# Optimization experiments

Measured on AMD Instinct MI355X. Metric: run time of the kernel, lower is better.

The kernel has to match this reference:

```python
import jax, jax.numpy as jnp
import numpy as np

B, C, L = 64, 128, 1024
SCALES = [8, 4, 2, 1]
EPS_BN = 1e-5


def _ema_vec(x_ds, alpha):
    # x_ds: [B, C, Ls]; alpha: [1, C, 1] in (0,1)
    Ls = x_ds.shape[-1]
    powers = jnp.arange(Ls - 1, -1, -1, dtype=x_ds.dtype)
    base = jnp.power(1.0 - alpha, powers)                                 # [1, C, Ls]
    w_num = jnp.concatenate([base[..., :1], base[..., 1:] * alpha], axis=-1)
    num = jnp.cumsum(x_ds * w_num, axis=-1)
    den = jnp.maximum(jnp.cumsum(base, axis=-1), 1e-12)
    return num / den


def _dwconv(x, w, s):
    # depthwise Conv1d: kernel 2s, stride s, pad s//2, groups=C, no bias
    return jax.lax.conv_general_dilated(
        x, w, window_strides=(s,), padding=[(s // 2, s // 2)],
        dimension_numbers=("NCH", "OIH", "NCH"), feature_group_count=C)


def _proj(v, w1, b1, w2, b2):
    # v: [B, C, Ls] -> Linear(Ls->L), exact GELU, Linear(L->L); torch Linear y = x @ W.T + b
    h = jax.nn.gelu(jnp.einsum("bcs,ls->bcl", v, w1) + b1, approximate=False)
    return jnp.einsum("bcl,ml->bcm", h, w2) + b2


def _hasd(x, bn_g, bn_b, branch, gate):
    Bn = x.shape[0]
    # BatchNorm1d over flattened (C*L) features, training-mode batch stats (biased var)
    v = x.reshape(Bn, C * L)
    mu = v.mean(axis=0)
    var = jnp.mean((v - mu) ** 2, axis=0)
    xn = (((v - mu) / jnp.sqrt(var + EPS_BN)) * bn_g + bn_b).reshape(Bn, C, L)
    trends, seasons, gates = [], [], []
    for s in SCALES:
        if s > 1:
            cw, w1, b1, w2, b2 = branch[s]
            down = _dwconv(xn, cw, s)                                     # [B, C, L//s]
            up = _proj(down, w1, b1, w2, b2)                              # [B, C, L]
        else:
            down = xn
            up = xn
        gw, gb, al = gate[s]
        alpha = jax.nn.sigmoid(al)
        trend_ds = _ema_vec(down, alpha)
        trend_up = _proj(trend_ds, w1, b1, w2, b2) if s > 1 else trend_ds
        season = up - trend_up
        trends.append(trend_up)
        seasons.append(season)
        gates.append(jax.nn.sigmoid(season.mean(axis=-1) @ gw.T + gb))    # [B, 1]
    g = jnp.concatenate(gates, axis=1)                                    # [B, n_scales]
    g = g / (g.sum(axis=1, keepdims=True) + 1e-6)
    g = g[:, :, None, None]
    trend_out = (jnp.stack(trends, axis=1) * g).sum(axis=1)
    season_out = (jnp.stack(seasons, axis=1) * g).sum(axis=1)
    return season_out, trend_out


def setup_inputs() -> dict:
    key = jax.random.key(0)
    ks = iter(jax.random.split(key, 64))
    d = {"x": jax.random.normal(next(ks), (B, C, L), jnp.float32)}
    d["bn_g"] = 1.0 + 0.1 * jax.random.normal(next(ks), (C * L,), jnp.float32)
    d["bn_b"] = 0.1 * jax.random.normal(next(ks), (C * L,), jnp.float32)
    for s in (8, 4, 2):
        Ls = L // s
        d[f"cw{s}"] = jax.random.normal(next(ks), (C, 1, 2 * s), jnp.float32) / np.sqrt(2 * s)
        d[f"w1_{s}"] = jax.random.normal(next(ks), (L, Ls), jnp.float32) / np.sqrt(Ls)
        d[f"b1_{s}"] = jnp.zeros((L,), jnp.float32)
        d[f"w2_{s}"] = jax.random.normal(next(ks), (L, L), jnp.float32) / np.sqrt(L)
        d[f"b2_{s}"] = jnp.zeros((L,), jnp.float32)
    for s in SCALES:
        d[f"gw{s}"] = jax.random.normal(next(ks), (1, C), jnp.float32) / np.sqrt(C)
        d[f"gb{s}"] = jnp.zeros((1,), jnp.float32)
        d[f"al{s}"] = jnp.full((1, C, 1), 0.3, jnp.float32)
    return d


def reference(x, bn_g, bn_b,
              cw8, w1_8, b1_8, w2_8, b2_8,
              cw4, w1_4, b1_4, w2_4, b2_4,
              cw2, w1_2, b1_2, w2_2, b2_2,
              gw8, gb8, al8, gw4, gb4, al4, gw2, gb2, al2, gw1, gb1, al1):
    branch = {8: (cw8, w1_8, b1_8, w2_8, b2_8),
              4: (cw4, w1_4, b1_4, w2_4, b2_4),
              2: (cw2, w1_2, b1_2, w2_2, b2_2)}
    gate = {8: (gw8, gb8, al8), 4: (gw4, gb4, al4),
            2: (gw2, gb2, al2), 1: (gw1, gb1, al1)}
    return _hasd(x, bn_g, bn_b, branch, gate)
```

## Files before the change

kernel.cpp:

```cpp
#include <hip/hip_runtime.h>
#include <hip/hip_bf16.h>
#include <math.h>

#define Bdim 64
#define Cdim 128
#define Ldim 1024
#define BC   (Bdim * Cdim)
#define CLn  (Cdim * Ldim)
#define TOT  (Bdim * CLn)

typedef unsigned short ushort_t;
typedef short s16x8 __attribute__((ext_vector_type(8)));
typedef float f32x4 __attribute__((ext_vector_type(4)));

__device__ __forceinline__ float bf2f(ushort_t u) {
    return __uint_as_float(((unsigned)u) << 16);
}
__device__ __forceinline__ ushort_t f2bf(float f) {
    __hip_bfloat16 h = __float2bfloat16(f);
    return *(ushort_t*)&h;
}
__device__ __forceinline__ void async16(const ushort_t* g, ushort_t* l) {
    __builtin_amdgcn_global_load_lds(
        (const __attribute__((address_space(1))) unsigned int*)g,
        (__attribute__((address_space(3))) unsigned int*)l, 16, 0, 0);
}
__device__ __forceinline__ float fast_gelu(float z) {
    float z2 = z * z;
    float inner = fmaf(0.044715f * z2, z, z);
    float e = __expf(-1.5957691216057308f * inner);
    return z * __builtin_amdgcn_rcpf(1.f + e);
}

__global__ __launch_bounds__(256) void bn_stats_kernel(
    const float* __restrict__ x, const float* __restrict__ bn_g,
    const float* __restrict__ bn_b, float* __restrict__ scale,
    float* __restrict__ shift)
{
    int f = blockIdx.x * 256 + threadIdx.x;
    float sum = 0.f, sumsq = 0.f;
    for (int b = 0; b < Bdim; ++b) {
        float v = x[(size_t)b * CLn + f];
        sum += v; sumsq += v * v;
    }
    float mu  = sum * (1.f / Bdim);
    float var = fmaxf(sumsq * (1.f / Bdim) - mu * mu, 0.f);
    float sc  = bn_g[f] / sqrtf(var + 1e-5f);
    scale[f] = sc;
    shift[f] = bn_b[f] - mu * sc;
}

__global__ __launch_bounds__(256) void convert_weights_kernel(
    const float* __restrict__ w1_8, const float* __restrict__ w1_4,
    const float* __restrict__ w1_2, const float* __restrict__ w2_8,
    const float* __restrict__ w2_4, const float* __restrict__ w2_2,
    ushort_t* __restrict__ dst)
{
    int idx = blockIdx.x * 256 + threadIdx.x;
    const float* src; int off;
    if      (idx < 131072)  { src = w1_8; off = 0; }
    else if (idx < 393216)  { src = w1_4; off = 131072; }
    else if (idx < 917504)  { src = w1_2; off = 393216; }
    else if (idx < 1966080) { src = w2_8; off = 917504; }
    else if (idx < 3014656) { src = w2_4; off = 1966080; }
    else                    { src = w2_2; off = 3014656; }
    dst[idx] = f2bf(src[idx - off]);
}

__global__ __launch_bounds__(256) void w2colsum_kernel(
    const float* __restrict__ w2_8, const float* __restrict__ w2_4,
    const float* __restrict__ w2_2, float* __restrict__ w2cs)
{
    const float* w = (blockIdx.y == 0) ? w2_8 : (blockIdx.y == 1) ? w2_4 : w2_2;
    int h  = blockIdx.x * 64 + (threadIdx.x & 63);
    int ls = threadIdx.x >> 6;
    float s = 0.f;
    for (int l = ls; l < 1024; l += 4) s += w[(size_t)l * 1024 + h];
    __shared__ float red[4][64];
    red[ls][threadIdx.x & 63] = s;
    __syncthreads();
    if (ls == 0)
        w2cs[blockIdx.y * 1024 + h] =
            red[0][threadIdx.x] + red[1][threadIdx.x] +
            red[2][threadIdx.x] + red[3][threadIdx.x];
}

__global__ __launch_bounds__(256) void ema_coef_kernel(
    const float* __restrict__ al1, const float* __restrict__ al2,
    const float* __restrict__ al4, const float* __restrict__ al8,
    float* __restrict__ coef, float* __restrict__ am)
{
    int c   = blockIdx.x;
    int tid = threadIdx.x;
    const float* als[4] = {al1, al2, al4, al8};
    const int Lss[4]    = {1024, 512, 256, 128};
    const int offs[4]   = {0, 1024, 1536, 1792};
#pragma unroll
    for (int si = 0; si < 4; ++si) {
        double a  = 1.0 / (1.0 + exp(-(double)als[si][c]));
        double m  = 1.0 - a;
        double lm = log(m);
        int Ls = Lss[si];
        for (int t = tid; t < Ls; t += 256) {
            double dt  = (1.0 - exp((double)(t + 1) * lm)) / a;
            double den = exp((double)(Ls - 1 - t) * lm) * dt;
            double ramp = (den >= 1e-12) ? 1.0 : den * 1e12;
            coef[(size_t)c * 1920 + offs[si] + t] = (float)(ramp / dt);
        }
        if (tid == 0) {
            am[c * 8 + si * 2 + 0] = (float)a;
            am[c * 8 + si * 2 + 1] = (float)m;
        }
    }
}

template<int SEG>
__device__ __forceinline__ void ema_pass1(
    const float* __restrict__ src, float a, float m, bool lead,
    float* __restrict__ xs, float& Sp, float& Sm)
{
    int lane = threadIdx.x & 63;
    if constexpr (SEG >= 4) {
#pragma unroll
        for (int i = 0; i < SEG; i += 4) {
            f32x4 u = *(const f32x4*)&src[lane * SEG + i];
            xs[i + 0] = u.x; xs[i + 1] = u.y;
            xs[i + 2] = u.z; xs[i + 3] = u.w;
        }
    } else {
        float2 u = *(const float2*)&src[lane * 2];
        xs[0] = u.x; xs[1] = u.y;
    }
    float p = 0.f;
#pragma unroll
    for (int i = 0; i < SEG; ++i) {
        float bi = a * xs[i];
        if (lead && lane == 0 && i == 0) bi = xs[0];
        p = fmaf(m, p, bi);
    }
    float sm = m;
#pragma unroll
    for (int i = 1; i < SEG; ++i) sm *= m;
    Sp = p; Sm = sm;
#pragma unroll
    for (int d = 1; d < 64; d <<= 1) {
        float pm = __shfl_up(Sp, d);
        float mm = __shfl_up(Sm, d);
        if (lane >= d) { Sp = fmaf(Sm, pm, Sp); Sm *= mm; }
    }
}

template<int SEG, bool DIFF>
__device__ __forceinline__ float ema_pass2(
    const float* __restrict__ xs, float a, float m, bool lead, float carry,
    const float* __restrict__ cf, ushort_t* __restrict__ dst)
{
    int lane = threadIdx.x & 63;
    float y = carry, diff = 0.f;
    unsigned pk[(SEG + 1) / 2];
#pragma unroll
    for (int i = 0; i < SEG; ++i) {
        float bi = a * xs[i];
        if (lead && lane == 0 && i == 0) bi = xs[0];
        y = fmaf(m, y, bi);
        float tr = y * cf[lane * SEG + i];
        unsigned h = f2bf(tr);
        if ((i & 1) == 0) pk[i >> 1] = h;
        else              pk[i >> 1] |= h << 16;
        if (DIFF) diff += xs[i] - tr;
    }
    if constexpr (SEG == 8) {
        uint4 v; v.x = pk[0]; v.y = pk[1]; v.z = pk[2]; v.w = pk[3];
        *(uint4*)(dst + lane * 8) = v;
    } else if constexpr (SEG == 4) {
        uint2 v; v.x = pk[0]; v.y = pk[1];
        *(uint2*)(dst + lane * 4) = v;
    } else {
        *(unsigned*)(dst + lane * 2) = pk[0];
    }
    return diff;
}

__global__ __launch_bounds__(256) void pre_kernel(
    const float* __restrict__ x, const float* __restrict__ scale,
    const float* __restrict__ shift,
    const float* __restrict__ cw8, const float* __restrict__ cw4,
    const float* __restrict__ cw2,
    const float* __restrict__ coef, const float* __restrict__ amtab,
    ushort_t* __restrict__ xn_bf, ushort_t* __restrict__ t1_bf,
    ushort_t* __restrict__ A8, ushort_t* __restrict__ A4,
    ushort_t* __restrict__ A2, float* __restrict__ rs)
{
    __shared__ float sxn[1024];
    __shared__ float sxnp[1056];
    __shared__ float sconv[896];
    __shared__ float sP0;
    __shared__ float sdiff[2];
    int r   = blockIdx.x;
    int c   = r & (Cdim - 1);
    int tid = threadIdx.x;

    {
        const float* xr = x + (size_t)r * 1024;
        float4 xv = *(const float4*)(xr + tid * 4);
        float4 sc = *(const float4*)(scale + (size_t)c * 1024 + tid * 4);
        float4 sh = *(const float4*)(shift + (size_t)c * 1024 + tid * 4);
        float v0 = fmaf(xv.x, sc.x, sh.x);
        float v1 = fmaf(xv.y, sc.y, sh.y);
        float v2 = fmaf(xv.z, sc.z, sh.z);
        float v3 = fmaf(xv.w, sc.w, sh.w);
        int p = tid * 4;
        sxn[p + 0] = v0; sxn[p + 1] = v1; sxn[p + 2] = v2; sxn[p + 3] = v3;
        int pp = p + (p >> 5);
        sxnp[pp + 0] = v0; sxnp[pp + 1] = v1;
        sxnp[pp + 2] = v2; sxnp[pp + 3] = v3;
        uint2 pk;
        pk.x = (unsigned)f2bf(v0) | ((unsigned)f2bf(v1) << 16);
        pk.y = (unsigned)f2bf(v2) | ((unsigned)f2bf(v3) << 16);
        *(uint2*)(xn_bf + (size_t)r * 1024 + tid * 4) = pk;
    }
    __syncthreads();

    {
        const float* w2 = cw2 + c * 4;
        unsigned a2pk = 0;
#pragma unroll
        for (int j = 0; j < 2; ++j) {
            int o = tid * 2 + j;
            int start = o * 2 - 1;
            float acc = 0.f;
#pragma unroll
            for (int k = 0; k < 4; ++k) {
                int pos = start + k;
                float v = (pos >= 0 && pos < 1024) ? sxnp[pos + (pos >> 5)] : 0.f;
                acc = fmaf(v, w2[k], acc);
            }
            sconv[o] = acc;
            a2pk |= ((unsigned)f2bf(acc)) << (j * 16);
        }
        *(unsigned*)(A2 + (size_t)r * 512 + tid * 2) = a2pk;
        {
            const float* w4 = cw4 + c * 8;
            int o = tid;
            int start = o * 4 - 2;
            float acc = 0.f;
#pragma unroll
            for (int k = 0; k < 8; ++k) {
                int pos = start + k;
                float v = (pos >= 0 && pos < 1024) ? sxnp[pos + (pos >> 5)] : 0.f;
                acc = fmaf(v, w4[k], acc);
            }
            sconv[512 + o] = acc;
            A4[(size_t)r * 256 + o] = f2bf(acc);
        }
        if (tid < 128) {
            const float* w8 = cw8 + c * 16;
            int o = tid;
            int start = o * 8 - 4;
            float acc = 0.f;
#pragma unroll
            for (int k = 0; k < 16; ++k) {
                int pos = start + k;
                float v = (pos >= 0 && pos < 1024) ? sxnp[pos + (pos >> 5)] : 0.f;
                acc = fmaf(v, w8[k], acc);
            }
            sconv[768 + o] = acc;
            A8[(size_t)r * 128 + o] = f2bf(acc);
        }
    }
    __syncthreads();

    int wave = tid >> 6;
    int lane = tid & 63;
    const float* cf = coef + (size_t)c * 1920;
    const float* am = amtab + c * 8;
    float xs[8];
    float Sp = 0.f, Sm = 1.f, aE = 0.f, mE = 0.f;

    if (wave == 0) {
        aE = am[0]; mE = am[1];
        ema_pass1<8>(sxn, aE, mE, true, xs, Sp, Sm);
        if (lane == 63) sP0 = Sp;
    } else if (wave == 1) {
        aE = am[0]; mE = am[1];
        ema_pass1<8>(sxn + 512, aE, mE, false, xs, Sp, Sm);
    } else if (wave == 2) {
        aE = am[2]; mE = am[3];
        ema_pass1<8>(sconv, aE, mE, true, xs, Sp, Sm);
    } else {
        aE = am[4]; mE = am[5];
        ema_pass1<4>(sconv + 512, aE, mE, true, xs, Sp, Sm);
    }
    __syncthreads();

    float cs  = __shfl_up(Sp, 1);
    float msf = __shfl_up(Sm, 1);
    float carry = lane ? cs : 0.f;

    if (wave == 0) {
        float d = ema_pass2<8, true>(xs, aE, mE, true, carry,
                                     cf, t1_bf + (size_t)r * 1024);
#pragma unroll
        for (int dd = 32; dd; dd >>= 1) d += __shfl_down(d, dd);
        if (lane == 0) sdiff[0] = d;
    } else if (wave == 1) {
        carry += sP0 * (lane ? msf : 1.f);
        float d = ema_pass2<8, true>(xs, aE, mE, false, carry,
                                     cf + 512, t1_bf + (size_t)r * 1024 + 512);
#pragma unroll
        for (int dd = 32; dd; dd >>= 1) d += __shfl_down(d, dd);
        if (lane == 0) sdiff[1] = d;
    } else if (wave == 2) {
        ema_pass2<8, false>(xs, aE, mE, true, carry,
                            cf + 1024, A2 + ((size_t)BC + r) * 512);
    } else {
        ema_pass2<4, false>(xs, aE, mE, true, carry,
                            cf + 1536, A4 + ((size_t)BC + r) * 256);
        float xs2[2];
        aE = am[6]; mE = am[7];
        ema_pass1<2>(sconv + 768, aE, mE, true, xs2, Sp, Sm);
        float cs2 = __shfl_up(Sp, 1);
        float c2  = lane ? cs2 : 0.f;
        ema_pass2<2, false>(xs2, aE, mE, true, c2,
                            cf + 1792, A8 + ((size_t)BC + r) * 128);
    }
    __syncthreads();
    if (tid == 0) rs[3 * BC + r] = sdiff[0] + sdiff[1];
}

__global__ __launch_bounds__(256, 2) void gemm1_kernel(
    const ushort_t* __restrict__ Abase,
    const ushort_t* __restrict__ Wbase,
    const float* __restrict__ b1_8, const float* __restrict__ b1_4,
    const float* __restrict__ b1_2, const float* __restrict__ w2cs,
    ushort_t* __restrict__ Hbase, float* __restrict__ rs)
{
    __shared__ ushort_t smem[24576];
    int gx = blockIdx.x;
    int z  = 2 - (gx >> 6);
    int mi = gx & 63;
    int K  = 128 << z;
    int NT = K >> 5;
    const ushort_t* A  = Abase + (size_t)2 * BC * 128 * ((1 << z) - 1);
    const ushort_t* Bw = Wbase + (size_t)131072 * ((1 << z) - 1);
    const float* bias  = (z == 0) ? b1_8 : (z == 1) ? b1_4 : b1_2;
    ushort_t* Hout     = Hbase + (size_t)z * 2 * TOT;

    int tid  = threadIdx.x;
    int wave = tid >> 6;
    int lane = tid & 63;
    int m0 = mi * 128, n0 = blockIdx.y * 128;
    int wm = (wave & 1) * 64, wn = (wave >> 1) * 64;
    int rlow = lane >> 2;
    int s4   = lane & 3;
    int fr   = lane & 15;
    int quad = lane >> 4;

    f32x4 accu[4][4], acct[4][4];
#pragma unroll
    for (int i = 0; i < 4; ++i)
#pragma unroll
        for (int j = 0; j < 4; ++j) {
            accu[i][j] = (f32x4){0.f, 0.f, 0.f, 0.f};
            acct[i][j] = (f32x4){0.f, 0.f, 0.f, 0.f};
        }

    auto stage = [&](int t, int buf) {
        int k0 = t * 32;
        ushort_t* base = smem + buf * 12288;
#pragma unroll
        for (int i = 0; i < 2; ++i) {
            int rb  = wave * 32 + i * 16;
            int row = rb + rlow;
            int cg  = (s4 - (row >> 1)) & 3;
            async16(A  + (size_t)(m0 + row) * K + k0 + cg * 8,      base + rb * 32);
            async16(A  + (size_t)(BC + m0 + row) * K + k0 + cg * 8, base + 4096 + rb * 32);
            async16(Bw + (size_t)(n0 + row) * K + k0 + cg * 8,      base + 8192 + rb * 32);
        }
    };

    stage(0, 0);
    int cur = 0;
    for (int t = 0; t < NT; ++t) {
        if (t + 1 < NT) {
            stage(t + 1, cur ^ 1);
            asm volatile("s_waitcnt vmcnt(6)" ::: "memory");
        } else {
            asm volatile("s_waitcnt vmcnt(0)" ::: "memory");
        }
        __builtin_amdgcn_s_barrier();
        __builtin_amdgcn_sched_barrier(0);
        const ushort_t* Au_ = smem + cur * 12288;
        const ushort_t* At_ = Au_ + 4096;
        const ushort_t* Bs_ = Au_ + 8192;
        s16x8 afu[4], aft[4], bfr[4];
#pragma unroll
        for (int q = 0; q < 4; ++q) {
            int nr = wn + q * 16 + fr;
            bfr[q] = *(const s16x8*)&Bs_[nr * 32 + ((quad + (nr >> 1)) & 3) * 8];
            int mr = wm + q * 16 + fr;
            afu[q] = *(const s16x8*)&Au_[mr * 32 + ((quad + (mr >> 1)) & 3) * 8];
            aft[q] = *(const s16x8*)&At_[mr * 32 + ((quad + (mr >> 1)) & 3) * 8];
        }
        __builtin_amdgcn_s_setprio(1);
#pragma unroll
        for (int mt = 0; mt < 4; ++mt)
#pragma unroll
            for (int nt = 0; nt < 4; ++nt)
                accu[mt][nt] = __builtin_amdgcn_mfma_f32_16x16x32_bf16(
                    afu[mt], bfr[nt], accu[mt][nt], 0, 0, 0);
#pragma unroll
        for (int mt = 0; mt < 4; ++mt)
#pragma unroll
            for (int nt = 0; nt < 4; ++nt)
                acct[mt][nt] = __builtin_amdgcn_mfma_f32_16x16x32_bf16(
                    aft[mt], bfr[nt], acct[mt][nt], 0, 0, 0);
        __builtin_amdgcn_s_setprio(0);
        __builtin_amdgcn_sched_barrier(0);
        __builtin_amdgcn_s_barrier();
        cur ^= 1;
    }

    float racc[16];
#pragma unroll
    for (int e = 0; e < 16; ++e) racc[e] = 0.f;
#pragma unroll
    for (int mt = 0; mt < 4; ++mt)
#pragma unroll
        for (int nt = 0; nt < 4; ++nt) {
            int col = n0 + wn + nt * 16 + fr;
            float bcol = bias[col];
            float wcs = w2cs[z * 1024 + col];
#pragma unroll
            for (int rr = 0; rr < 4; ++rr) {
                size_t row = m0 + wm + mt * 16 + quad * 4 + rr;
                float gu = fast_gelu(accu[mt][nt][rr] + bcol);
                float gt = fast_gelu(acct[mt][nt][rr] + bcol);
                Hout[row * 1024 + col]        = f2bf(gu);
                Hout[(BC + row) * 1024 + col] = f2bf(gt);
                racc[mt * 4 + rr] = fmaf(gu - gt, wcs, racc[mt * 4 + rr]);
            }
        }
#pragma unroll
    for (int e = 0; e < 16; ++e) {
        float v = racc[e];
        v += __shfl_xor(v, 1); v += __shfl_xor(v, 2);
        v += __shfl_xor(v, 4); v += __shfl_xor(v, 8);
        if (fr == 0) {
            int mt = e >> 2, rr = e & 3;
            int row = m0 + wm + mt * 16 + quad * 4 + rr;
            atomicAdd(&rs[z * BC + row], v);
        }
    }
}

__global__ __launch_bounds__(256, 2) void gemm2_kernel(
    const ushort_t* __restrict__ Hbase,
    const ushort_t* __restrict__ W2base,
    const float* __restrict__ b2_8, const float* __restrict__ b2_4,
    const float* __restrict__ b2_2, const float* __restrict__ g,
    const ushort_t* __restrict__ t1_bf, const ushort_t* __restrict__ xn_bf,
    float* __restrict__ trend_out, float* __restrict__ season_out)
{
    __shared__ ushort_t smem[24576];
    int tid  = threadIdx.x;
    int wave = tid >> 6;
    int lane = tid & 63;
    int m0 = blockIdx.x * 128, n0 = blockIdx.y * 128;
    int wm = (wave & 1) * 64, wn = (wave >> 1) * 64;
    int rlow = lane >> 2;
    int s4   = lane & 3;
    int fr   = lane & 15;
    int quad = lane >> 4;
    int b = m0 >> 7;
    float gv0 = g[b * 4 + 0], gv1 = g[b * 4 + 1], gv2 = g[b * 4 + 2];
    float g1  = g[b * 4 + 3];
    float gsv[3] = {gv0, gv1, gv2};

    f32x4 accu[4][4], acct[4][4];
#pragma unroll
    for (int i = 0; i < 4; ++i)
#pragma unroll
        for (int j = 0; j < 4; ++j) {
            accu[i][j] = (f32x4){0.f, 0.f, 0.f, 0.f};
            acct[i][j] = (f32x4){0.f, 0.f, 0.f, 0.f};
        }

    auto stage = [&](int kt, int buf) {
        int s  = kt >> 5;
        int k0 = (kt & 31) * 32;
        const ushort_t* Au = Hbase + (size_t)s * 2 * TOT;
        const ushort_t* At = Au + TOT;
        const ushort_t* Bw = W2base + (size_t)s * 1048576;
        ushort_t* base = smem + buf * 12288;
#pragma unroll
        for (int i = 0; i < 2; ++i) {
            int rb  = wave * 32 + i * 16;
            int row = rb + rlow;
            int cg  = (s4 - (row >> 1)) & 3;
            size_t goff = (size_t)(m0 + row) * 1024 + k0 + cg * 8;
            async16(Au + goff, base + rb * 32);
            async16(At + goff, base + 4096 + rb * 32);
            async16(Bw + (size_t)(n0 + row) * 1024 + k0 + cg * 8,
                    base + 8192 + rb * 32);
        }
    };

    stage(0, 0);
    int cur = 0;
    for (int kt = 0; kt < 96; ++kt) {
        if (kt + 1 < 96) {
            stage(kt + 1, cur ^ 1);
            asm volatile("s_waitcnt vmcnt(6)" ::: "memory");
        } else {
            asm volatile("s_waitcnt vmcnt(0)" ::: "memory");
        }
        __builtin_amdgcn_s_barrier();
        __builtin_amdgcn_sched_barrier(0);
        if (kt > 0 && (kt & 31) == 0) {
            int s = kt >> 5;
            float rr_ = gsv[s - 1] / fmaxf(gsv[s], 1e-30f);
#pragma unroll
            for (int mt = 0; mt < 4; ++mt)
#pragma unroll
                for (int nt = 0; nt < 4; ++nt)
#pragma unroll
                    for (int rr = 0; rr < 4; ++rr) {
                        accu[mt][nt][rr] *= rr_;
                        acct[mt][nt][rr] *= rr_;
                    }
        }
        const ushort_t* Au_ = smem + cur * 12288;
        const ushort_t* At_ = Au_ + 4096;
        const ushort_t* Bs_ = Au_ + 8192;
        s16x8 afu[4], aft[4], bfr[4];
#pragma unroll
        for (int q = 0; q < 4; ++q) {
            int nr = wn + q * 16 + fr;
            bfr[q] = *(const s16x8*)&Bs_[nr * 32 + ((quad + (nr >> 1)) & 3) * 8];
            int mr = wm + q * 16 + fr;
            afu[q] = *(const s16x8*)&Au_[mr * 32 + ((quad + (mr >> 1)) & 3) * 8];
            aft[q] = *(const s16x8*)&At_[mr * 32 + ((quad + (mr >> 1)) & 3) * 8];
        }
        __builtin_amdgcn_s_setprio(1);
#pragma unroll
        for (int mt = 0; mt < 4; ++mt)
#pragma unroll
            for (int nt = 0; nt < 4; ++nt)
                accu[mt][nt] = __builtin_amdgcn_mfma_f32_16x16x32_bf16(
                    afu[mt], bfr[nt], accu[mt][nt], 0, 0, 0);
#pragma unroll
        for (int mt = 0; mt < 4; ++mt)
#pragma unroll
            for (int nt = 0; nt < 4; ++nt)
                acct[mt][nt] = __builtin_amdgcn_mfma_f32_16x16x32_bf16(
                    aft[mt], bfr[nt], acct[mt][nt], 0, 0, 0);
        __builtin_amdgcn_s_setprio(0);
        __builtin_amdgcn_sched_barrier(0);
        __builtin_amdgcn_s_barrier();
        cur ^= 1;
    }
#pragma unroll
    for (int mt = 0; mt < 4; ++mt)
#pragma unroll
        for (int nt = 0; nt < 4; ++nt)
#pragma unroll
            for (int rr = 0; rr < 4; ++rr) {
                accu[mt][nt][rr] *= gv2;
                acct[mt][nt][rr] *= gv2;
            }

#pragma unroll
    for (int mt = 0; mt < 4; ++mt)
#pragma unroll
        for (int nt = 0; nt < 4; ++nt) {
            int col = n0 + wn + nt * 16 + fr;
            float cb2 = gv0 * b2_8[col] + gv1 * b2_4[col] + gv2 * b2_2[col];
#pragma unroll
            for (int r = 0; r < 4; ++r) {
                size_t row = m0 + wm + mt * 16 + quad * 4 + r;
                size_t idx = row * 1024 + col;
                float tr = acct[mt][nt][r] + cb2 + g1 * bf2f(t1_bf[idx]);
                float se = accu[mt][nt][r] + cb2 + g1 * bf2f(xn_bf[idx]) - tr;
                trend_out[idx]  = tr;
                season_out[idx] = se;
            }
        }
}

__global__ __launch_bounds__(128) void gate_kernel(
    const float* __restrict__ rs,
    const float* __restrict__ gw8, const float* __restrict__ gb8,
    const float* __restrict__ gw4, const float* __restrict__ gb4,
    const float* __restrict__ gw2, const float* __restrict__ gb2,
    const float* __restrict__ gw1, const float* __restrict__ gb1,
    float* __restrict__ g)
{
    int b = blockIdx.x;
    int c = threadIdx.x;
    const float* gws[4] = {gw8, gw4, gw2, gw1};
    const float* gbs[4] = {gb8, gb4, gb2, gb1};
    __shared__ float buf[128];
    __shared__ float gates[4];
    for (int si = 0; si < 4; ++si) {
        buf[c] = rs[si * BC + b * Cdim + c] * (1.f / Ldim) * gws[si][c];
        __syncthreads();
        for (int off = 64; off >= 1; off >>= 1) {
            if (c < off) buf[c] += buf[c + off];
            __syncthreads();
        }
        if (c == 0) {
            float z = buf[0] + gbs[si][0];
            gates[si] = 1.f / (1.f + expf(-z));
        }
        __syncthreads();
    }
    if (c == 0) {
        float s = gates[0] + gates[1] + gates[2] + gates[3] + 1e-6f;
#pragma unroll
        for (int si = 0; si < 4; ++si) g[b * 4 + si] = gates[si] / s;
    }
}

extern "C" void kernel_launch(void* const* d_in, const int* in_sizes, int n_in,
                              void* d_out, int out_size, void* d_ws, size_t ws_size,
                              hipStream_t stream)
{
    const float* x    = (const float*)d_in[0];
    const float* bn_g = (const float*)d_in[1];
    const float* bn_b = (const float*)d_in[2];
    const float* cw8  = (const float*)d_in[3];
    const float* w1_8 = (const float*)d_in[4];
    const float* b1_8 = (const float*)d_in[5];
    const float* w2_8 = (const float*)d_in[6];
    const float* b2_8 = (const float*)d_in[7];
    const float* cw4  = (const float*)d_in[8];
    const float* w1_4 = (const float*)d_in[9];
    const float* b1_4 = (const float*)d_in[10];
    const float* w2_4 = (const float*)d_in[11];
    const float* b2_4 = (const float*)d_in[12];
    const float* cw2  = (const float*)d_in[13];
    const float* w1_2 = (const float*)d_in[14];
    const float* b1_2 = (const float*)d_in[15];
    const float* w2_2 = (const float*)d_in[16];
    const float* b2_2 = (const float*)d_in[17];
    const float* gw8  = (const float*)d_in[18];
    const float* gb8  = (const float*)d_in[19];
    const float* al8  = (const float*)d_in[20];
    const float* gw4  = (const float*)d_in[21];
    const float* gb4  = (const float*)d_in[22];
    const float* al4  = (const float*)d_in[23];
    const float* gw2  = (const float*)d_in[24];
    const float* gb2  = (const float*)d_in[25];
    const float* al2  = (const float*)d_in[26];
    const float* gw1  = (const float*)d_in[27];
    const float* gb1  = (const float*)d_in[28];
    const float* al1  = (const float*)d_in[29];

    ushort_t* p_xn  = (ushort_t*)d_ws;
    ushort_t* p_t1  = p_xn + TOT;
    ushort_t* p_H   = p_t1 + TOT;
    ushort_t* p_wb  = p_H + 6 * (size_t)TOT;
    ushort_t* p_w1b = p_wb;
    ushort_t* p_w2b = p_wb + 917504;
    float*    p_sc  = (float*)(p_wb + 4063232);
    float*    p_sh  = p_sc + CLn;
    float*    p_w2cs = p_sh + CLn;
    float*    p_rs  = p_w2cs + 3 * 1024;
    float*    p_g   = p_rs + 4 * BC;
    float*    p_coef = (float*)p_H;
    float*    p_am   = p_coef + 128 * 1920;
    ushort_t* p_A8 = (ushort_t*)d_out;
    ushort_t* p_A4 = p_A8 + 2 * (size_t)BC * 128;
    ushort_t* p_A2 = p_A4 + 2 * (size_t)BC * 256;
    float*    p_season = (float*)d_out;
    float*    p_trend  = (float*)d_out + TOT;

    hipMemsetAsync(p_rs, 0, 4 * BC * sizeof(float), stream);
    bn_stats_kernel<<<CLn / 256, 256, 0, stream>>>(x, bn_g, bn_b, p_sc, p_sh);
    ema_coef_kernel<<<128, 256, 0, stream>>>(al1, al2, al4, al8, p_coef, p_am);
    convert_weights_kernel<<<4063232 / 256, 256, 0, stream>>>(
        w1_8, w1_4, w1_2, w2_8, w2_4, w2_2, p_wb);
    w2colsum_kernel<<<dim3(16, 3), 256, 0, stream>>>(w2_8, w2_4, w2_2, p_w2cs);

    pre_kernel<<<BC, 256, 0, stream>>>(x, p_sc, p_sh, cw8, cw4, cw2,
                                       p_coef, p_am,
                                       p_xn, p_t1, p_A8, p_A4, p_A2, p_rs);

    gemm1_kernel<<<dim3(192, 8), 256, 0, stream>>>(
        p_A8, p_w1b, b1_8, b1_4, b1_2, p_w2cs, p_H, p_rs);

    gate_kernel<<<Bdim, 128, 0, stream>>>(p_rs, gw8, gb8, gw4, gb4,
                                          gw2, gb2, gw1, gb1, p_g);

    gemm2_kernel<<<dim3(64, 8), 256, 0, stream>>>(
        p_H, p_w2b, b2_8, b2_4, b2_2, p_g, p_t1, p_xn, p_trend, p_season);
}
```

Before: 434.5 us.

## Load GEMM A-operand fragments straight from global into registers, stage only B in LDS

Both GEMM kernels stop staging the A operands (u and t activations) through LDS. Each wave now loads its MFMA fragments directly from global memory into registers, two steps ahead, and only the shared weight tile B goes through async LDS copies. LDS use drops from 48KB to 16KB per block and the A-tile LDS reads are removed. In exchange, A reads hit global memory without reuse across waves (the two N-waves load the same rows), the kernel holds more registers for double-buffered fragments, and the vmcnt wait logic becomes more fragile.

```diff
diff --git a/kernel.cpp b/kernel.cpp
--- a/kernel.cpp
+++ b/kernel.cpp
@@ -328,6 +328,41 @@
     if (tid == 0) rs[3 * BC + r] = sdiff[0] + sdiff[1];
 }
 
+#define MFMA_STEP(Bsbase, FU, FT)                                              \
+    {                                                                          \
+        const ushort_t* Bs_ = (Bsbase);                                        \
+        s16x8 bfr[4];                                                          \
+        _Pragma("unroll")                                                      \
+        for (int q = 0; q < 4; ++q) {                                          \
+            int nr = wn + q * 16 + fr;                                         \
+            bfr[q] = *(const s16x8*)&Bs_[nr * 32 + ((quad + (nr >> 1)) & 3) * 8]; \
+        }                                                                      \
+        __builtin_amdgcn_s_setprio(1);                                         \
+        _Pragma("unroll")                                                      \
+        for (int mt = 0; mt < 4; ++mt)                                         \
+            _Pragma("unroll")                                                  \
+            for (int nt = 0; nt < 4; ++nt)                                     \
+                accu[mt][nt] = __builtin_amdgcn_mfma_f32_16x16x32_bf16(        \
+                    FU[mt], bfr[nt], accu[mt][nt], 0, 0, 0);                   \
+        _Pragma("unroll")                                                      \
+        for (int mt = 0; mt < 4; ++mt)                                         \
+            _Pragma("unroll")                                                  \
+            for (int nt = 0; nt < 4; ++nt)                                     \
+                acct[mt][nt] = __builtin_amdgcn_mfma_f32_16x16x32_bf16(        \
+                    FT[mt], bfr[nt], acct[mt][nt], 0, 0, 0);                   \
+        __builtin_amdgcn_s_setprio(0);                                         \
+        __builtin_amdgcn_sched_barrier(0);                                     \
+        __builtin_amdgcn_s_barrier();                                          \
+    }
+
+#define WAIT_ENTER(w10)                                                        \
+    {                                                                          \
+        if (w10) { asm volatile("s_waitcnt vmcnt(10)" ::: "memory"); }         \
+        else     { asm volatile("s_waitcnt vmcnt(0)"  ::: "memory"); }         \
+        __builtin_amdgcn_s_barrier();                                          \
+        __builtin_amdgcn_sched_barrier(0);                                     \
+    }
+
 __global__ __launch_bounds__(256, 2) void gemm1_kernel(
     const ushort_t* __restrict__ Abase,
     const ushort_t* __restrict__ Wbase,
@@ -335,7 +370,7 @@
     const float* __restrict__ b1_2, const float* __restrict__ w2cs,
     ushort_t* __restrict__ Hbase, float* __restrict__ rs)
 {
-    __shared__ ushort_t smem[24576];
+    __shared__ ushort_t smem[8192];
     int gx = blockIdx.x;
     int z  = 2 - (gx >> 6);
     int mi = gx & 63;
@@ -365,60 +400,44 @@
             acct[i][j] = (f32x4){0.f, 0.f, 0.f, 0.f};
         }
 
-    auto stage = [&](int t, int buf) {
-        int k0 = t * 32;
-        ushort_t* base = smem + buf * 12288;
-#pragma unroll
-        for (int i = 0; i < 2; ++i) {
-            int rb  = wave * 32 + i * 16;
-            int row = rb + rlow;
-            int cg  = (s4 - (row >> 1)) & 3;
-            async16(A  + (size_t)(m0 + row) * K + k0 + cg * 8,      base + rb * 32);
-            async16(A  + (size_t)(BC + m0 + row) * K + k0 + cg * 8, base + 4096 + rb * 32);
-            async16(Bw + (size_t)(n0 + row) * K + k0 + cg * 8,      base + 8192 + rb * 32);
-        }
-    };
-
-    stage(0, 0);
-    int cur = 0;
-    for (int t = 0; t < NT; ++t) {
-        if (t + 1 < NT) {
-            stage(t + 1, cur ^ 1);
-            asm volatile("s_waitcnt vmcnt(6)" ::: "memory");
-        } else {
-            asm volatile("s_waitcnt vmcnt(0)" ::: "memory");
-        }
-        __builtin_amdgcn_s_barrier();
+#define G1_STAGE_B(step, buf)                                                  \
+    {                                                                          \
+        int k0_ = (step) * 32;                                                 \
+        ushort_t* base_ = smem + (buf) * 4096;                                 \
+        _Pragma("unroll")                                                      \
+        for (int i = 0; i < 2; ++i) {                                          \
+            int rb  = wave * 32 + i * 16;                                      \
+            int row = rb + rlow;                                               \
+            int cg  = (s4 - (row >> 1)) & 3;                                   \
+            async16(Bw + (size_t)(n0 + row) * K + k0_ + cg * 8, base_ + rb * 32); \
+        }                                                                      \
+    }
+#define G1_LOAD_A(step, FU, FT)                                                \
+    {                                                                          \
+        int k0_ = (step) * 32;                                                 \
+        _Pragma("unroll")                                                      \
+        for (int q = 0; q < 4; ++q) {                                          \
+            int mr = wm + q * 16 + fr;                                         \
+            size_t ofU = (size_t)(m0 + mr) * K + k0_ + quad * 8;               \
+            FU[q] = *(const s16x8*)(A + ofU);                                  \
+            FT[q] = *(const s16x8*)(A + (size_t)BC * K + ofU);                 \
+        }                                                                      \
+    }
+
+    s16x8 afu0[4], aft0[4], afu1[4], aft1[4];
+    G1_STAGE_B(0, 0); G1_LOAD_A(0, afu0, aft0);
+    G1_STAGE_B(1, 1); G1_LOAD_A(1, afu1, aft1);
+    __builtin_amdgcn_sched_barrier(0);
+
+    for (int t = 0; t < NT; t += 2) {
+        WAIT_ENTER(t + 1 < NT);
+        MFMA_STEP(smem, afu0, aft0);
+        if (t + 2 < NT) { G1_STAGE_B(t + 2, 0); G1_LOAD_A(t + 2, afu0, aft0); }
         __builtin_amdgcn_sched_barrier(0);
-        const ushort_t* Au_ = smem + cur * 12288;
-        const ushort_t* At_ = Au_ + 4096;
-        const ushort_t* Bs_ = Au_ + 8192;
-        s16x8 afu[4], aft[4], bfr[4];
-#pragma unroll
-        for (int q = 0; q < 4; ++q) {
-            int nr = wn + q * 16 + fr;
-            bfr[q] = *(const s16x8*)&Bs_[nr * 32 + ((quad + (nr >> 1)) & 3) * 8];
-            int mr = wm + q * 16 + fr;
-            afu[q] = *(const s16x8*)&Au_[mr * 32 + ((quad + (mr >> 1)) & 3) * 8];
-            aft[q] = *(const s16x8*)&At_[mr * 32 + ((quad + (mr >> 1)) & 3) * 8];
-        }
-        __builtin_amdgcn_s_setprio(1);
-#pragma unroll
-        for (int mt = 0; mt < 4; ++mt)
-#pragma unroll
-            for (int nt = 0; nt < 4; ++nt)
-                accu[mt][nt] = __builtin_amdgcn_mfma_f32_16x16x32_bf16(
-                    afu[mt], bfr[nt], accu[mt][nt], 0, 0, 0);
-#pragma unroll
-        for (int mt = 0; mt < 4; ++mt)
-#pragma unroll
-            for (int nt = 0; nt < 4; ++nt)
-                acct[mt][nt] = __builtin_amdgcn_mfma_f32_16x16x32_bf16(
-                    aft[mt], bfr[nt], acct[mt][nt], 0, 0, 0);
-        __builtin_amdgcn_s_setprio(0);
+        WAIT_ENTER(t + 2 < NT);
+        MFMA_STEP(smem + 4096, afu1, aft1);
+        if (t + 3 < NT) { G1_STAGE_B(t + 3, 1); G1_LOAD_A(t + 3, afu1, aft1); }
         __builtin_amdgcn_sched_barrier(0);
-        __builtin_amdgcn_s_barrier();
-        cur ^= 1;
     }
 
     float racc[16];
@@ -452,6 +471,8 @@
             atomicAdd(&rs[z * BC + row], v);
         }
     }
+#undef G1_STAGE_B
+#undef G1_LOAD_A
 }
 
 __global__ __launch_bounds__(256, 2) void gemm2_kernel(
@@ -462,7 +483,7 @@
     const ushort_t* __restrict__ t1_bf, const ushort_t* __restrict__ xn_bf,
     float* __restrict__ trend_out, float* __restrict__ season_out)
 {
-    __shared__ ushort_t smem[24576];
+    __shared__ ushort_t smem[8192];
     int tid  = threadIdx.x;
     int wave = tid >> 6;
     int lane = tid & 63;
@@ -486,37 +507,41 @@
             acct[i][j] = (f32x4){0.f, 0.f, 0.f, 0.f};
         }
 
-    auto stage = [&](int kt, int buf) {
-        int s  = kt >> 5;
-        int k0 = (kt & 31) * 32;
-        const ushort_t* Au = Hbase + (size_t)s * 2 * TOT;
-        const ushort_t* At = Au + TOT;
-        const ushort_t* Bw = W2base + (size_t)s * 1048576;
-        ushort_t* base = smem + buf * 12288;
-#pragma unroll
-        for (int i = 0; i < 2; ++i) {
-            int rb  = wave * 32 + i * 16;
-            int row = rb + rlow;
-            int cg  = (s4 - (row >> 1)) & 3;
-            size_t goff = (size_t)(m0 + row) * 1024 + k0 + cg * 8;
-            async16(Au + goff, base + rb * 32);
-            async16(At + goff, base + 4096 + rb * 32);
-            async16(Bw + (size_t)(n0 + row) * 1024 + k0 + cg * 8,
-                    base + 8192 + rb * 32);
-        }
-    };
-
-    stage(0, 0);
-    int cur = 0;
-    for (int kt = 0; kt < 96; ++kt) {
-        if (kt + 1 < 96) {
-            stage(kt + 1, cur ^ 1);
-            asm volatile("s_waitcnt vmcnt(6)" ::: "memory");
-        } else {
-            asm volatile("s_waitcnt vmcnt(0)" ::: "memory");
-        }
-        __builtin_amdgcn_s_barrier();
-        __builtin_amdgcn_sched_barrier(0);
+#define G2_STAGE_B(step, buf)                                                  \
+    {                                                                          \
+        int s_  = (step) >> 5;                                                 \
+        int k0_ = ((step) & 31) * 32;                                          \
+        const ushort_t* Bw_ = W2base + (size_t)s_ * 1048576;                   \
+        ushort_t* base_ = smem + (buf) * 4096;                                 \
+        _Pragma("unroll")                                                      \
+        for (int i = 0; i < 2; ++i) {                                          \
+            int rb  = wave * 32 + i * 16;                                      \
+            int row = rb + rlow;                                               \
+            int cg  = (s4 - (row >> 1)) & 3;                                   \
+            async16(Bw_ + (size_t)(n0 + row) * 1024 + k0_ + cg * 8,            \
+                    base_ + rb * 32);                                          \
+        }                                                                      \
+    }
+#define G2_LOAD_A(step, FU, FT)                                                \
+    {                                                                          \
+        int s_  = (step) >> 5;                                                 \
+        int k0_ = ((step) & 31) * 32;                                          \
+        const ushort_t* Au_ = Hbase + (size_t)s_ * 2 * TOT;                    \
+        _Pragma("unroll")                                                      \
+        for (int q = 0; q < 4; ++q) {                                          \
+            int mr = wm + q * 16 + fr;                                         \
+            size_t of_ = (size_t)(m0 + mr) * 1024 + k0_ + quad * 8;            \
+            FU[q] = *(const s16x8*)(Au_ + of_);                                \
+            FT[q] = *(const s16x8*)(Au_ + TOT + of_);                          \
+        }                                                                      \
+    }
+
+    s16x8 afu0[4], aft0[4], afu1[4], aft1[4];
+    G2_STAGE_B(0, 0); G2_LOAD_A(0, afu0, aft0);
+    G2_STAGE_B(1, 1); G2_LOAD_A(1, afu1, aft1);
+    __builtin_amdgcn_sched_barrier(0);
+
+    for (int kt = 0; kt < 96; kt += 2) {
         if (kt > 0 && (kt & 31) == 0) {
             int s = kt >> 5;
             float rr_ = gsv[s - 1] / fmaxf(gsv[s], 1e-30f);
@@ -530,35 +555,14 @@
                         acct[mt][nt][rr] *= rr_;
                     }
         }
-        const ushort_t* Au_ = smem + cur * 12288;
-        const ushort_t* At_ = Au_ + 4096;
-        const ushort_t* Bs_ = Au_ + 8192;
-        s16x8 afu[4], aft[4], bfr[4];
-#pragma unroll
-        for (int q = 0; q < 4; ++q) {
-            int nr = wn + q * 16 + fr;
-            bfr[q] = *(const s16x8*)&Bs_[nr * 32 + ((quad + (nr >> 1)) & 3) * 8];
-            int mr = wm + q * 16 + fr;
-            afu[q] = *(const s16x8*)&Au_[mr * 32 + ((quad + (mr >> 1)) & 3) * 8];
-            aft[q] = *(const s16x8*)&At_[mr * 32 + ((quad + (mr >> 1)) & 3) * 8];
-        }
-        __builtin_amdgcn_s_setprio(1);
-#pragma unroll
-        for (int mt = 0; mt < 4; ++mt)
-#pragma unroll
-            for (int nt = 0; nt < 4; ++nt)
-                accu[mt][nt] = __builtin_amdgcn_mfma_f32_16x16x32_bf16(
-                    afu[mt], bfr[nt], accu[mt][nt], 0, 0, 0);
-#pragma unroll
-        for (int mt = 0; mt < 4; ++mt)
-#pragma unroll
-            for (int nt = 0; nt < 4; ++nt)
-                acct[mt][nt] = __builtin_amdgcn_mfma_f32_16x16x32_bf16(
-                    aft[mt], bfr[nt], acct[mt][nt], 0, 0, 0);
-        __builtin_amdgcn_s_setprio(0);
+        WAIT_ENTER(kt + 1 < 96);
+        MFMA_STEP(smem, afu0, aft0);
+        if (kt + 2 < 96) { G2_STAGE_B(kt + 2, 0); G2_LOAD_A(kt + 2, afu0, aft0); }
         __builtin_amdgcn_sched_barrier(0);
-        __builtin_amdgcn_s_barrier();
-        cur ^= 1;
+        WAIT_ENTER(kt + 2 < 96);
+        MFMA_STEP(smem + 4096, afu1, aft1);
+        if (kt + 3 < 96) { G2_STAGE_B(kt + 3, 1); G2_LOAD_A(kt + 3, afu1, aft1); }
+        __builtin_amdgcn_sched_barrier(0);
     }
 #pragma unroll
     for (int mt = 0; mt < 4; ++mt)
@@ -586,6 +590,8 @@
                 season_out[idx] = se;
             }
         }
+#undef G2_STAGE_B
+#undef G2_LOAD_A
 }
 
 __global__ __launch_bounds__(128) void gate_kernel(
```

Result: slower. 585.9 us (+34.8%).
